# Optimization experiments

Measured on AMD Instinct MI355X. Metric: run time of the kernel, lower is better.

Reference implementation:

```python
import jax, jax.numpy as jnp
import numpy as np

B, H, W, C = 64, 32, 32, 256
HZ, WZ = 16, 16
N = 64          # hidden_dim = n_proposals
K = 3           # dynamic depthwise kernel size
EPS = 1e-5


def _layernorm(x, g, b):
    mu = jnp.mean(x, axis=-1, keepdims=True)
    var = jnp.var(x, axis=-1, keepdims=True)
    return (x - mu) * jax.lax.rsqrt(var + EPS) * g + b


def setup_inputs() -> dict:
    key = jax.random.key(0)
    ks = jax.random.split(key, 8)
    s = 0.02  # weight init scale
    return {
        "x_feat": jax.random.normal(ks[0], (B, H, W, C), jnp.float32),
        "z_feat": jax.random.normal(ks[1], (B, HZ, WZ, C), jnp.float32),
        "Wz": jax.random.normal(ks[2], (C, N), jnp.float32) * s,
        "bz": jnp.zeros((N,), jnp.float32),
        "Wx": jax.random.normal(ks[3], (C, N), jnp.float32) * s,
        "bx": jnp.zeros((N,), jnp.float32),
        "Wdyn": jax.random.normal(ks[4], (C, N + K), jnp.float32) * s,
        "bdyn": jnp.zeros((N + K,), jnp.float32),
        "g_norm": jnp.ones((C,), jnp.float32),
        "b_norm": jnp.zeros((C,), jnp.float32),
        "Wp": jax.random.normal(ks[5], (C, 1), jnp.float32) * s,
        "bp": jnp.zeros((1,), jnp.float32),
        "g_ln": jnp.ones((C,), jnp.float32),
        "b_ln": jnp.zeros((C,), jnp.float32),
    }


def _dysep_conv_atten(query, value, Wdyn, bdyn, g_norm, b_norm):
    # query, value: [B, N, C]
    dy = query @ Wdyn + bdyn                      # [B, N, N+K]
    w_depth = dy[:, :, :K]                        # [B, N, K] per-channel depthwise kernels
    w_point = dy[:, :, K:]                        # [B, N, N] per-sample pointwise (1x1) weights
    # depthwise conv along C with 'same' padding (torch conv1d = cross-correlation)
    vpad = jnp.pad(value, ((0, 0), (0, 0), (1, 1)))
    depth = (w_depth[..., 0:1] * vpad[:, :, 0:C]
             + w_depth[..., 1:2] * vpad[:, :, 1:C + 1]
             + w_depth[..., 2:3] * vpad[:, :, 2:C + 2])
    depth = jax.nn.relu(depth)                    # [B, N, C]
    point = jnp.einsum('bnm,bmc->bnc', w_point, depth)
    return _layernorm(point, g_norm, b_norm)


def reference(x_feat, z_feat, Wz, bz, Wx, bx, Wdyn, bdyn,
              g_norm, b_norm, Wp, bp, g_ln, b_ln):
    # kernels from template features (detached in the original: kernels.detach())
    z_core = z_feat @ Wz + bz                                   # [B,HZ,WZ,N]
    kernels = jnp.einsum('bhwn,bhwc->bnc', z_core, z_feat)      # [B,N,C]
    kernels = jax.lax.stop_gradient(kernels)

    x_n = x_feat @ Wx + bx                                      # [B,H,W,N]
    kernels_x = jnp.einsum('bhwn,bhwc->bnc', x_n, x_feat)       # [B,N,C]
    kernels_x = _dysep_conv_atten(kernels, kernels_x, Wdyn, bdyn, g_norm, b_norm)

    x_corr = jnp.einsum('bnc,bhwn->bhwc', kernels_x, x_n)       # [B,H,W,C]
    proto = kernels_x @ Wp + bp                                 # [B,N,1]
    tem = jax.nn.sigmoid(jnp.einsum('bnd,bnc->bdc', proto, kernels_x))  # [B,1,C]
    tem = tem[:, :, None, :]                                    # [B,1,1,C]
    x_corr = x_corr * tem

    return x_feat + jax.nn.relu(_layernorm(x_corr, g_ln, b_ln))
```

## Files before the change

kernel.cpp:

```cpp
#include <hip/hip_runtime.h>
#include <math.h>

#define EPSV 1e-5f

typedef __attribute__((ext_vector_type(8))) short short8;
typedef __attribute__((ext_vector_type(4))) float f32x4;

static __device__ __forceinline__ unsigned bfpack2(float lo, float hi) {
    union { float f; unsigned u; } a, b;
    a.f = lo; b.f = hi;
    unsigned ua = a.u + 0x7fffu + ((a.u >> 16) & 1u);
    unsigned ub = b.u + 0x7fffu + ((b.u >> 16) & 1u);
    return (ua >> 16) | (ub & 0xffff0000u);
}

__global__ __launch_bounds__(256) void gram(
    const float* __restrict__ Xx, const float* __restrict__ Xz,
    float* __restrict__ Gx, float* __restrict__ Gz,
    float* __restrict__ csx, float* __restrict__ csz)
{
    __shared__ __align__(16) unsigned short AT[64 * 72];
    __shared__ __align__(16) unsigned short BT[64 * 72];
    __shared__ float csr[256];
    int id = blockIdx.x;
    const float* X; float* G; float* cs; int P;
    if (id < 1024) { X = Xx; G = Gx; cs = csx; P = 1024; }
    else { id -= 1024; X = Xz; G = Gz; cs = csz; P = 256; }
    const int b = id & 63;
    const int tile = id >> 6;
    const int ci = tile >> 2, cj = tile & 3;
    const int nk = P >> 6;
    const int t = threadIdx.x;
    const int cl = t & 63, ph = t >> 6;
    const int w = t >> 6, quad = (t >> 4) & 3, lane16 = t & 15;
    const float* Xb = X + (long)b * P * 256;
    const float* Acol = Xb + ci * 64 + cl;
    const float* Bcol = Xb + cj * 64 + cl;
    const bool diag = (ci == cj);

    f32x4 acc[4] = {{0.f,0.f,0.f,0.f},{0.f,0.f,0.f,0.f},{0.f,0.f,0.f,0.f},{0.f,0.f,0.f,0.f}};
    float csum = 0.f;

    for (int kc = 0; kc < nk; ++kc) {
        const int p0 = kc * 64 + ph * 16;
        float va[16], vb[16];
#pragma unroll
        for (int k = 0; k < 16; ++k) va[k] = Acol[(long)(p0 + k) * 256];
        if (!diag) {
#pragma unroll
            for (int k = 0; k < 16; ++k) vb[k] = Bcol[(long)(p0 + k) * 256];
        } else {
#pragma unroll
            for (int k = 0; k < 16; ++k) { vb[k] = va[k]; csum += va[k]; }
        }
        uint4 a0, a1, b0, b1;
        a0.x = bfpack2(va[0], va[1]);   a0.y = bfpack2(va[2], va[3]);
        a0.z = bfpack2(va[4], va[5]);   a0.w = bfpack2(va[6], va[7]);
        a1.x = bfpack2(va[8], va[9]);   a1.y = bfpack2(va[10], va[11]);
        a1.z = bfpack2(va[12], va[13]); a1.w = bfpack2(va[14], va[15]);
        b0.x = bfpack2(vb[0], vb[1]);   b0.y = bfpack2(vb[2], vb[3]);
        b0.z = bfpack2(vb[4], vb[5]);   b0.w = bfpack2(vb[6], vb[7]);
        b1.x = bfpack2(vb[8], vb[9]);   b1.y = bfpack2(vb[10], vb[11]);
        b1.z = bfpack2(vb[12], vb[13]); b1.w = bfpack2(vb[14], vb[15]);
        __syncthreads();
        *(uint4*)&AT[cl * 72 + ph * 16]     = a0;
        *(uint4*)&AT[cl * 72 + ph * 16 + 8] = a1;
        *(uint4*)&BT[cl * 72 + ph * 16]     = b0;
        *(uint4*)&BT[cl * 72 + ph * 16 + 8] = b1;
        __syncthreads();
#pragma unroll
        for (int ks = 0; ks < 2; ++ks) {
            const int ko = ks * 32 + quad * 8;
            short8 bfrag = *(const short8*)&BT[(w * 16 + lane16) * 72 + ko];
#pragma unroll
            for (int mi = 0; mi < 4; ++mi) {
                short8 afrag = *(const short8*)&AT[(mi * 16 + lane16) * 72 + ko];
                acc[mi] = __builtin_amdgcn_mfma_f32_16x16x32_bf16(afrag, bfrag, acc[mi], 0, 0, 0);
            }
        }
    }
#pragma unroll
    for (int mi = 0; mi < 4; ++mi) {
        long row = (long)(b * 256 + ci * 64 + mi * 16 + quad * 4);
        int col = cj * 64 + w * 16 + lane16;
#pragma unroll
        for (int r = 0; r < 4; ++r)
            G[(row + r) * 256 + col] = acc[mi][r];
    }
    if (diag) {
        csr[ph * 64 + cl] = csum;
        __syncthreads();
        if (t < 64)
            cs[b * 256 + ci * 64 + t] = csr[t] + csr[64 + t] + csr[128 + t] + csr[192 + t];
    }
}

__global__ __launch_bounds__(256) void proj(
    const float* __restrict__ Gx, const float* __restrict__ csx,
    const float* __restrict__ Wx, const float* __restrict__ bx,
    float* __restrict__ kxr,
    const float* __restrict__ Gz, const float* __restrict__ csz,
    const float* __restrict__ Wz, const float* __restrict__ bz,
    float* __restrict__ kern)
{
    __shared__ __align__(16) unsigned short ATW[64 * 264];
    __shared__ __align__(16) unsigned short BTC[64 * 72];
    const int t = threadIdx.x;
    const int id = blockIdx.x;
    const int b = id & 63, s = id >> 6;
    const float *G, *cs, *W, *bias; float* O;
    if (s < 4) { G = Gx; cs = csx; W = Wx; bias = bx; O = kxr; }
    else       { G = Gz; cs = csz; W = Wz; bias = bz; O = kern; }
    const int ct = s & 3;
    const int n = t & 63, ph = t >> 6;
#pragma unroll
    for (int cc = 0; cc < 4; ++cc) {
        float v[16];
#pragma unroll
        for (int k = 0; k < 16; ++k) v[k] = W[(ph * 64 + cc * 16 + k) * 64 + n];
        uint4 p0, p1;
        p0.x = bfpack2(v[0], v[1]);   p0.y = bfpack2(v[2], v[3]);
        p0.z = bfpack2(v[4], v[5]);   p0.w = bfpack2(v[6], v[7]);
        p1.x = bfpack2(v[8], v[9]);   p1.y = bfpack2(v[10], v[11]);
        p1.z = bfpack2(v[12], v[13]); p1.w = bfpack2(v[14], v[15]);
        *(uint4*)&ATW[n * 264 + ph * 64 + cc * 16]     = p0;
        *(uint4*)&ATW[n * 264 + ph * 64 + cc * 16 + 8] = p1;
    }
    const int row = t >> 2, cq = t & 3;
    const int w = t >> 6, quad = (t >> 4) & 3, lane16 = t & 15;
    const float* Grow = G + ((long)(b * 256 + ct * 64 + row)) * 256 + cq * 16;
    f32x4 acc[4] = {{0.f,0.f,0.f,0.f},{0.f,0.f,0.f,0.f},{0.f,0.f,0.f,0.f},{0.f,0.f,0.f,0.f}};
    for (int kc = 0; kc < 4; ++kc) {
        float4 g0 = *(const float4*)(Grow + kc * 64 + 0);
        float4 g1 = *(const float4*)(Grow + kc * 64 + 4);
        float4 g2 = *(const float4*)(Grow + kc * 64 + 8);
        float4 g3 = *(const float4*)(Grow + kc * 64 + 12);
        uint4 pk0, pk1;
        pk0.x = bfpack2(g0.x, g0.y); pk0.y = bfpack2(g0.z, g0.w);
        pk0.z = bfpack2(g1.x, g1.y); pk0.w = bfpack2(g1.z, g1.w);
        pk1.x = bfpack2(g2.x, g2.y); pk1.y = bfpack2(g2.z, g2.w);
        pk1.z = bfpack2(g3.x, g3.y); pk1.w = bfpack2(g3.z, g3.w);
        __syncthreads();
        *(uint4*)&BTC[row * 72 + cq * 16]     = pk0;
        *(uint4*)&BTC[row * 72 + cq * 16 + 8] = pk1;
        __syncthreads();
#pragma unroll
        for (int ks = 0; ks < 2; ++ks) {
            const int ko = ks * 32 + quad * 8;
            short8 bfrag = *(const short8*)&BTC[(w * 16 + lane16) * 72 + ko];
#pragma unroll
            for (int mi = 0; mi < 4; ++mi) {
                short8 afrag = *(const short8*)&ATW[(mi * 16 + lane16) * 264 + kc * 64 + ko];
                acc[mi] = __builtin_amdgcn_mfma_f32_16x16x32_bf16(afrag, bfrag, acc[mi], 0, 0, 0);
            }
        }
    }
    const int col = ct * 64 + w * 16 + lane16;
    const float csv = cs[b * 256 + col];
#pragma unroll
    for (int mi = 0; mi < 4; ++mi) {
        const int nrow = mi * 16 + quad * 4;
#pragma unroll
        for (int r = 0; r < 4; ++r)
            O[((long)(b * 64 + nrow + r)) * 256 + col] = acc[mi][r] + bias[nrow + r] * csv;
    }
}

__global__ __launch_bounds__(256) void dy_all(
    const float* __restrict__ kern, const float* __restrict__ Wdyn,
    const float* __restrict__ bdyn, float* __restrict__ dyb)
{
    __shared__ float Ac[16 * 64];
    __shared__ float Wc[16 * 64];
    __shared__ float Wd3[48];
    const int b = blockIdx.x, t = threadIdx.x;
    const int tr = t >> 4, tc = t & 15;
    float acc[4][4];
#pragma unroll
    for (int j = 0; j < 4; ++j) {
        float bj = bdyn[3 + tc * 4 + j];
        acc[0][j] = bj; acc[1][j] = bj; acc[2][j] = bj; acc[3][j] = bj;
    }
    const int lr = t >> 2, lc = (t & 3) * 4;
    const int wl = t >> 4, wj = (t & 15) * 4;
    const int nwd = t / 3, jwd = t - nwd * 3;
    float wdacc = 0.f;
    float4 av = *(const float4*)(kern + ((long)(b * 64 + lr)) * 256 + lc);
    float w0 = Wdyn[wl * 67 + 3 + wj + 0];
    float w1 = Wdyn[wl * 67 + 3 + wj + 1];
    float w2 = Wdyn[wl * 67 + 3 + wj + 2];
    float w3 = Wdyn[wl * 67 + 3 + wj + 3];
    float wdr = (t < 48) ? Wdyn[(t / 3) * 67 + (t % 3)] : 0.f;

    for (int c0 = 0; c0 < 256; c0 += 16) {
        Ac[(lc+0)*64 + lr] = av.x; Ac[(lc+1)*64 + lr] = av.y;
        Ac[(lc+2)*64 + lr] = av.z; Ac[(lc+3)*64 + lr] = av.w;
        Wc[wl*64 + wj+0] = w0; Wc[wl*64 + wj+1] = w1;
        Wc[wl*64 + wj+2] = w2; Wc[wl*64 + wj+3] = w3;
        if (t < 48) Wd3[t] = wdr;
        __syncthreads();
        if (c0 + 16 < 256) {
            av = *(const float4*)(kern + ((long)(b * 64 + lr)) * 256 + c0 + 16 + lc);
            w0 = Wdyn[(c0 + 16 + wl) * 67 + 3 + wj + 0];
            w1 = Wdyn[(c0 + 16 + wl) * 67 + 3 + wj + 1];
            w2 = Wdyn[(c0 + 16 + wl) * 67 + 3 + wj + 2];
            w3 = Wdyn[(c0 + 16 + wl) * 67 + 3 + wj + 3];
            if (t < 48) wdr = Wdyn[(c0 + 16 + t / 3) * 67 + (t % 3)];
        }
#pragma unroll
        for (int cl = 0; cl < 16; ++cl) {
            float4 a = *(float4*)&Ac[cl * 64 + tr * 4];
            float4 w = *(float4*)&Wc[cl * 64 + tc * 4];
            acc[0][0]+=a.x*w.x; acc[0][1]+=a.x*w.y; acc[0][2]+=a.x*w.z; acc[0][3]+=a.x*w.w;
            acc[1][0]+=a.y*w.x; acc[1][1]+=a.y*w.y; acc[1][2]+=a.y*w.z; acc[1][3]+=a.y*w.w;
            acc[2][0]+=a.z*w.x; acc[2][1]+=a.z*w.y; acc[2][2]+=a.z*w.z; acc[2][3]+=a.z*w.w;
            acc[3][0]+=a.w*w.x; acc[3][1]+=a.w*w.y; acc[3][2]+=a.w*w.z; acc[3][3]+=a.w*w.w;
        }
        if (t < 192) {
#pragma unroll
            for (int cl = 0; cl < 16; ++cl)
                wdacc += Ac[cl * 64 + nwd] * Wd3[cl * 3 + jwd];
        }
        __syncthreads();
    }
#pragma unroll
    for (int i = 0; i < 4; ++i) {
        float4 o = make_float4(acc[i][0], acc[i][1], acc[i][2], acc[i][3]);
        *(float4*)(dyb + ((long)(b * 64 + tr * 4 + i)) * 68 + tc * 4) = o;
    }
    if (t < 192) dyb[((long)(b * 64 + nwd)) * 68 + 64 + jwd] = wdacc + bdyn[jwd];
}

__global__ __launch_bounds__(256) void depthpoint(
    const float* __restrict__ dyb, const float* __restrict__ v,
    const float* __restrict__ g, const float* __restrict__ Wp,
    float* __restrict__ point, float* __restrict__ partials)
{
    __shared__ float smem[13312];
    float* wpT = smem;
    float* wd3 = smem + 4352;
    float* vt  = smem + 4608;
    float* dep = smem + 8960;
    float* rs  = vt;

    const int t = threadIdx.x;
    const int b = blockIdx.y, ct = blockIdx.x, c0 = ct * 64;
    const int tr = t >> 4, tc = t & 15;

#pragma unroll
    for (int i = 0; i < 4; ++i) {
        int idx = t + i * 256; int n = idx >> 4, m0 = (idx & 15) * 4;
        float4 w4 = *(const float4*)(dyb + ((long)(b * 64 + n)) * 68 + m0);
        wpT[(m0+0)*68 + n] = w4.x; wpT[(m0+1)*68 + n] = w4.y;
        wpT[(m0+2)*68 + n] = w4.z; wpT[(m0+3)*68 + n] = w4.w;
    }
    if (t < 64) {
        long o = ((long)(b * 64 + t)) * 68 + 64;
        wd3[t*4+0] = dyb[o+0]; wd3[t*4+1] = dyb[o+1]; wd3[t*4+2] = dyb[o+2];
    }
    {
        int m = t >> 2, lc0 = (t & 3) * 17;
#pragma unroll
        for (int k = 0; k < 17; ++k) {
            int lc = lc0 + k;
            if (lc < 66) {
                int c = c0 - 1 + lc;
                vt[m * 68 + lc] = (c >= 0 && c < 256) ? v[((long)(b * 64 + m)) * 256 + c] : 0.f;
            }
        }
    }
    __syncthreads();
#pragma unroll
    for (int im = 0; im < 4; ++im) {
        int m = tr * 4 + im;
        float w0 = wd3[m*4+0], w1 = wd3[m*4+1], w2 = wd3[m*4+2];
#pragma unroll
        for (int jc = 0; jc < 4; ++jc) {
            int cl = tc * 4 + jc;
            float d = w0 * vt[m*68 + cl] + w1 * vt[m*68 + cl + 1] + w2 * vt[m*68 + cl + 2];
            dep[m*68 + cl] = fmaxf(d, 0.f);
        }
    }
    __syncthreads();
    float acc[4][4] = {};
#pragma unroll 16
    for (int m = 0; m < 64; ++m) {
        float4 a4 = *(float4*)&wpT[m * 68 + tr * 4];
        float4 d4 = *(float4*)&dep[m * 68 + tc * 4];
        acc[0][0]+=a4.x*d4.x; acc[0][1]+=a4.x*d4.y; acc[0][2]+=a4.x*d4.z; acc[0][3]+=a4.x*d4.w;
        acc[1][0]+=a4.y*d4.x; acc[1][1]+=a4.y*d4.y; acc[1][2]+=a4.y*d4.z; acc[1][3]+=a4.y*d4.w;
        acc[2][0]+=a4.z*d4.x; acc[2][1]+=a4.z*d4.y; acc[2][2]+=a4.z*d4.z; acc[2][3]+=a4.z*d4.w;
        acc[3][0]+=a4.w*d4.x; acc[3][1]+=a4.w*d4.y; acc[3][2]+=a4.w*d4.z; acc[3][3]+=a4.w*d4.w;
    }
    int cg = c0 + tc * 4;
    float4 g4  = *(const float4*)(g + cg);
    float4 wp4 = *(const float4*)(Wp + cg);
    float gw0 = g4.x*wp4.x, gw1 = g4.y*wp4.y, gw2 = g4.z*wp4.z, gw3 = g4.w*wp4.w;
#pragma unroll
    for (int i = 0; i < 4; ++i) {
        float4 o = make_float4(acc[i][0], acc[i][1], acc[i][2], acc[i][3]);
        *(float4*)(point + ((long)(b * 64 + tr * 4 + i)) * 256 + cg) = o;
        float s  = o.x + o.y + o.z + o.w;
        float s2 = o.x*o.x + o.y*o.y + o.z*o.z + o.w*o.w;
        float dg = o.x*gw0 + o.y*gw1 + o.z*gw2 + o.w*gw3;
        rs[0*1088 + (tr*4+i)*17 + tc] = s;
        rs[1*1088 + (tr*4+i)*17 + tc] = s2;
        rs[2*1088 + (tr*4+i)*17 + tc] = dg;
    }
    __syncthreads();
    if (t < 64) {
        float s = 0.f, s2 = 0.f, dg = 0.f;
#pragma unroll
        for (int j = 0; j < 16; ++j) {
            s  += rs[t*17 + j];
            s2 += rs[1088 + t*17 + j];
            dg += rs[2176 + t*17 + j];
        }
        long base = ((long)(b * 4 + ct)) * 192;
        partials[base + t]        = s;
        partials[base + 64 + t]   = s2;
        partials[base + 128 + t]  = dg;
    }
}

__global__ __launch_bounds__(256) void lntem(
    const float* __restrict__ partials, const float* __restrict__ point,
    const float* __restrict__ g, const float* __restrict__ bta,
    const float* __restrict__ Wp, const float* __restrict__ bp,
    float* __restrict__ murr, float* __restrict__ AB)
{
    __shared__ float sA[256], sB[256];
    __shared__ float wnv[64];
    __shared__ float tot[4];
    const int b = blockIdx.x, t = threadIdx.x;
    const int c = t;
    float gc = g[c], bc = bta[c], wpc = Wp[c];
    sA[t] = gc * wpc; sB[t] = bc * wpc;
    __syncthreads();
    for (int off = 128; off >= 1; off >>= 1) {
        if (t < off) { sA[t] += sA[t+off]; sB[t] += sB[t+off]; }
        __syncthreads();
    }
    if (t == 0) { tot[0] = sA[0]; tot[1] = sB[0] + bp[0]; }
    __syncthreads();
    float Sgw = tot[0], Sbw = tot[1];

    float protoe = 0.f, mu = 0.f, rr = 0.f;
    if (t < 64) {
        float S1 = 0.f, S2 = 0.f, Sdg = 0.f;
#pragma unroll
        for (int ct = 0; ct < 4; ++ct) {
            long o = ((long)(b * 4 + ct)) * 192;
            S1 += partials[o + t]; S2 += partials[o + 64 + t]; Sdg += partials[o + 128 + t];
        }
        mu = S1 * (1.f / 256.f);
        float var = S2 * (1.f / 256.f) - mu * mu;
        rr = rsqrtf(var + EPSV);
        protoe = rr * (Sdg - mu * Sgw) + Sbw;
        wnv[t] = protoe * rr;
        murr[b * 128 + 2*t]     = rr;
        murr[b * 128 + 2*t + 1] = -mu * rr;
    }
    __syncthreads();
    sA[t] = (t < 64) ? protoe * rr * mu : 0.f;
    sB[t] = (t < 64) ? protoe : 0.f;
    __syncthreads();
    for (int off = 128; off >= 1; off >>= 1) {
        if (t < off) { sA[t] += sA[t+off]; sB[t] += sB[t+off]; }
        __syncthreads();
    }
    if (t == 0) { tot[2] = sA[0]; tot[3] = sB[0]; }
    __syncthreads();
    float Bv = tot[2], Sv = tot[3];

    const float* pcol = point + (long)b * 64 * 256 + c;
    float a0 = 0.f, a1 = 0.f, a2 = 0.f, a3 = 0.f;
#pragma unroll
    for (int n = 0; n < 64; n += 4) {
        a0 += wnv[n+0] * pcol[(n+0) * 256];
        a1 += wnv[n+1] * pcol[(n+1) * 256];
        a2 += wnv[n+2] * pcol[(n+2) * 256];
        a3 += wnv[n+3] * pcol[(n+3) * 256];
    }
    float accA = a0 + a1 + a2 + a3;
    float x = gc * (accA - Bv) + bc * Sv;
    float temv = 1.f / (1.f + expf(-x));
    AB[b * 512 + c]       = gc * temv;
    AB[b * 512 + 256 + c] = bc * temv;
}

__global__ __launch_bounds__(256) void buildM(
    const float* __restrict__ point, const float* __restrict__ murr,
    const float* __restrict__ AB, const float* __restrict__ Wx,
    const float* __restrict__ bx,
    unsigned short* __restrict__ MT, float* __restrict__ svec)
{
    __shared__ float ks_s[64 * 68];
    __shared__ float wt_s[64 * 68];
    const int t = threadIdx.x;
    const int id = blockIdx.x;
    const int b = id & 63, mt = id >> 6;
    {
        const int n = t >> 2, q = t & 3;
        const float rn = murr[b * 128 + 2 * n], qn = murr[b * 128 + 2 * n + 1];
        const float* prow = point + ((long)(b * 64 + n)) * 256 + mt * 64 + q * 16;
        const float* Arow = AB + b * 512 + mt * 64 + q * 16;
#pragma unroll
        for (int j = 0; j < 4; ++j) {
            float4 p4 = *(const float4*)(prow + j * 4);
            float4 A4 = *(const float4*)(Arow + j * 4);
            float4 B4 = *(const float4*)(Arow + 256 + j * 4);
            float4 kv;
            kv.x = (p4.x * rn + qn) * A4.x + B4.x;
            kv.y = (p4.y * rn + qn) * A4.y + B4.y;
            kv.z = (p4.z * rn + qn) * A4.z + B4.z;
            kv.w = (p4.w * rn + qn) * A4.w + B4.w;
            *(float4*)&ks_s[n * 68 + q * 16 + j * 4] = kv;
        }
    }
    __syncthreads();
    if (t < 64) {
        float sv = 0.f;
#pragma unroll
        for (int n2 = 0; n2 < 64; ++n2) sv += bx[n2] * ks_s[n2 * 68 + t];
        svec[b * 256 + mt * 64 + t] = sv;
    }
    const int tr = t >> 4, tc = t & 15;
    const int nw = t & 63, ph = t >> 6;
    for (int cc = 0; cc < 4; ++cc) {
        float wv[16];
#pragma unroll
        for (int k = 0; k < 16; ++k) wv[k] = Wx[(cc * 64 + ph * 16 + k) * 64 + nw];
        __syncthreads();
#pragma unroll
        for (int k = 0; k < 16; ++k) wt_s[nw * 68 + ph * 16 + k] = wv[k];
        __syncthreads();
        float a2[4][4] = {};
#pragma unroll 16
        for (int n2 = 0; n2 < 64; ++n2) {
            float4 a4 = *(float4*)&ks_s[n2 * 68 + tr * 4];
            float4 w4 = *(float4*)&wt_s[n2 * 68 + tc * 4];
            a2[0][0]+=a4.x*w4.x; a2[0][1]+=a4.x*w4.y; a2[0][2]+=a4.x*w4.z; a2[0][3]+=a4.x*w4.w;
            a2[1][0]+=a4.y*w4.x; a2[1][1]+=a4.y*w4.y; a2[1][2]+=a4.y*w4.z; a2[1][3]+=a4.y*w4.w;
            a2[2][0]+=a4.z*w4.x; a2[2][1]+=a4.z*w4.y; a2[2][2]+=a4.z*w4.z; a2[2][3]+=a4.z*w4.w;
            a2[3][0]+=a4.w*w4.x; a2[3][1]+=a4.w*w4.y; a2[3][2]+=a4.w*w4.z; a2[3][3]+=a4.w*w4.w;
        }
#pragma unroll
        for (int i = 0; i < 4; ++i) {
            uint2 pk;
            pk.x = bfpack2(a2[i][0], a2[i][1]);
            pk.y = bfpack2(a2[i][2], a2[i][3]);
            *(uint2*)&MT[((long)(b * 256 + mt * 64 + tr * 4 + i)) * 256 + cc * 64 + tc * 4] = pk;
        }
    }
}

__global__ __launch_bounds__(256) void final2(
    const float* __restrict__ xf, const unsigned short* __restrict__ MT,
    const float* __restrict__ svec, const float* __restrict__ g,
    const float* __restrict__ bt, float* __restrict__ out)
{
    __shared__ __align__(16) float SlArr[64 * 132];
    __shared__ float red1[256], red2[256];
    __shared__ float muS[64], rrS[64];
    unsigned short* XT = (unsigned short*)SlArr;
    float* Sl = SlArr;
    const int t = threadIdx.x;
    const int id = blockIdx.x;
    const int b = id & 63, pt = id >> 6;
    const int w = t >> 6, quad = (t >> 4) & 3, lane16 = t & 15;
    const float* Xb = xf + ((long)(b * 1024 + pt * 64)) * 256;
    {
        const int p = t >> 2, q = t & 3;
#pragma unroll
        for (int j = 0; j < 4; ++j)
#pragma unroll
            for (int i = 0; i < 4; ++i) {
                const int c = j * 64 + q * 16 + i * 4;
                float4 v = *(const float4*)(Xb + (long)p * 256 + c);
                uint2 pk;
                pk.x = bfpack2(v.x, v.y);
                pk.y = bfpack2(v.z, v.w);
                *(uint2*)&XT[p * 264 + c] = pk;
            }
    }
    __syncthreads();
    f32x4 acc[4][4] = {};
    const unsigned short* Mb = MT + (long)b * 65536;
    for (int ks = 0; ks < 8; ++ks) {
        const int ko = ks * 32 + quad * 8;
        short8 bf4[4], af4[4];
#pragma unroll
        for (int ni = 0; ni < 4; ++ni)
            bf4[ni] = *(const short8*)(Mb + (long)(w * 64 + ni * 16 + lane16) * 256 + ko);
#pragma unroll
        for (int mi = 0; mi < 4; ++mi)
            af4[mi] = *(const short8*)&XT[(mi * 16 + lane16) * 264 + ko];
#pragma unroll
        for (int mi = 0; mi < 4; ++mi)
#pragma unroll
            for (int ni = 0; ni < 4; ++ni)
                acc[mi][ni] = __builtin_amdgcn_mfma_f32_16x16x32_bf16(af4[mi], bf4[ni], acc[mi][ni], 0, 0, 0);
    }
    float sv4[4];
#pragma unroll
    for (int ni = 0; ni < 4; ++ni) sv4[ni] = svec[b * 256 + w * 64 + ni * 16 + lane16];
#pragma unroll
    for (int mi = 0; mi < 4; ++mi)
#pragma unroll
        for (int r = 0; r < 4; ++r) {
            float s1 = 0.f, s2 = 0.f;
#pragma unroll
            for (int ni = 0; ni < 4; ++ni) {
                float v = acc[mi][ni][r] + sv4[ni];
                acc[mi][ni][r] = v;
                s1 += v; s2 += v * v;
            }
#pragma unroll
            for (int m = 1; m <= 8; m <<= 1) {
                s1 += __shfl_xor(s1, m);
                s2 += __shfl_xor(s2, m);
            }
            if (lane16 == 0) {
                red1[(mi * 16 + quad * 4 + r) * 4 + w] = s1;
                red2[(mi * 16 + quad * 4 + r) * 4 + w] = s2;
            }
        }
    __syncthreads();
    if (t < 64) {
        float sa = red1[t*4] + red1[t*4+1] + red1[t*4+2] + red1[t*4+3];
        float sb = red2[t*4] + red2[t*4+1] + red2[t*4+2] + red2[t*4+3];
        float m = sa * (1.f / 256.f);
        muS[t] = m;
        rrS[t] = rsqrtf(sb * (1.f / 256.f) - m * m + EPSV);
    }
#pragma unroll
    for (int h = 0; h < 2; ++h) {
        __syncthreads();
        if ((w >> 1) == h) {
            const int chalf = (w & 1) * 64;
#pragma unroll
            for (int mi = 0; mi < 4; ++mi)
#pragma unroll
                for (int ni = 0; ni < 4; ++ni)
#pragma unroll
                    for (int r = 0; r < 4; ++r)
                        Sl[(mi * 16 + quad * 4 + r) * 132 + chalf + ni * 16 + lane16] = acc[mi][ni][r];
        }
        __syncthreads();
        {
            const int p = t >> 2, q = t & 3;
            const float m = muS[p], rr = rrS[p];
            const long grow = ((long)(b * 1024 + pt * 64 + p)) * 256;
#pragma unroll
            for (int j = 0; j < 8; ++j) {
                const int cl = q * 32 + j * 4;
                const int c = h * 128 + cl;
                float4 a  = *(float4*)&Sl[p * 132 + cl];
                float4 g4 = *(const float4*)(g + c);
                float4 b4 = *(const float4*)(bt + c);
                float4 xv = *(const float4*)(xf + grow + c);
                float4 o;
                o.x = xv.x + fmaxf((a.x - m) * rr * g4.x + b4.x, 0.f);
                o.y = xv.y + fmaxf((a.y - m) * rr * g4.y + b4.y, 0.f);
                o.z = xv.z + fmaxf((a.z - m) * rr * g4.z + b4.z, 0.f);
                o.w = xv.w + fmaxf((a.w - m) * rr * g4.w + b4.w, 0.f);
                *(float4*)(out + grow + c) = o;
            }
        }
    }
}

extern "C" void kernel_launch(void* const* d_in, const int* in_sizes, int n_in,
                              void* d_out, int out_size, void* d_ws, size_t ws_size,
                              hipStream_t stream)
{
    (void)in_sizes; (void)n_in; (void)out_size; (void)ws_size;
    const float* x_feat = (const float*)d_in[0];
    const float* z_feat = (const float*)d_in[1];
    const float* Wz     = (const float*)d_in[2];
    const float* bz     = (const float*)d_in[3];
    const float* Wx     = (const float*)d_in[4];
    const float* bx     = (const float*)d_in[5];
    const float* Wdyn   = (const float*)d_in[6];
    const float* bdyn   = (const float*)d_in[7];
    const float* g_norm = (const float*)d_in[8];
    const float* b_norm = (const float*)d_in[9];
    const float* Wp     = (const float*)d_in[10];
    const float* bp     = (const float*)d_in[11];
    const float* g_ln   = (const float*)d_in[12];
    const float* b_ln   = (const float*)d_in[13];
    float* out = (float*)d_out;

    float* ws       = (float*)d_ws;
    float* Gx       = ws;
    float* Gz       = Gx + 4194304;
    float* kern     = Gz + 4194304;
    float* kxr      = kern + 1048576;
    float* point    = kxr + 1048576;
    float* dyb      = point + 1048576;
    float* partials = dyb + 278528;
    float* murr     = partials + 49152;
    float* AB       = murr + 8192;
    float* csx      = AB + 32768;
    float* csz      = csx + 16384;
    float* svec     = csz + 16384;
    unsigned short* MT = (unsigned short*)(svec + 16384);

    gram<<<2048, 256, 0, stream>>>(x_feat, z_feat, Gx, Gz, csx, csz);
    proj<<<512, 256, 0, stream>>>(Gx, csx, Wx, bx, kxr, Gz, csz, Wz, bz, kern);
    dy_all<<<64, 256, 0, stream>>>(kern, Wdyn, bdyn, dyb);
    depthpoint<<<dim3(4, 64), 256, 0, stream>>>(dyb, kxr, g_norm, Wp, point, partials);
    lntem<<<64, 256, 0, stream>>>(partials, point, g_norm, b_norm, Wp, bp, murr, AB);
    buildM<<<256, 256, 0, stream>>>(point, murr, AB, Wx, bx, MT, svec);
    final2<<<1024, 256, 0, stream>>>(x_feat, MT, svec, g_ln, b_ln, out);
}
```

Baseline: 299.2 us.

## Exploit Gram symmetry with larger 128x128 tiles and halve final2 row tile

The Gram kernel now computes 128x128 tiles and only the three upper-triangular blocks per batch, mirroring the off-diagonal block into the lower half. Loads switch from strided scalar column reads to row-wise float4 loads. This removes the redundant work on symmetric blocks and reduces memory traffic. The final kernel processes 32 rows per block instead of 64 and launches twice as many blocks, trading per-block MFMA reuse of MT for more parallelism and less LDS per block. The mirrored transposed store is uncoalesced.

```diff
diff --git a/kernel.cpp b/kernel.cpp
--- a/kernel.cpp
+++ b/kernel.cpp
@@ -19,79 +19,111 @@
     float* __restrict__ Gx, float* __restrict__ Gz,
     float* __restrict__ csx, float* __restrict__ csz)
 {
-    __shared__ __align__(16) unsigned short AT[64 * 72];
-    __shared__ __align__(16) unsigned short BT[64 * 72];
-    __shared__ float csr[256];
+    __shared__ __align__(16) unsigned short AT[128 * 72];
+    __shared__ __align__(16) unsigned short BT[128 * 72];
+    __shared__ float csr[8 * 128];
     int id = blockIdx.x;
     const float* X; float* G; float* cs; int P;
-    if (id < 1024) { X = Xx; G = Gx; cs = csx; P = 1024; }
-    else { id -= 1024; X = Xz; G = Gz; cs = csz; P = 256; }
+    if (id < 192) { X = Xx; G = Gx; cs = csx; P = 1024; }
+    else { id -= 192; X = Xz; G = Gz; cs = csz; P = 256; }
     const int b = id & 63;
     const int tile = id >> 6;
-    const int ci = tile >> 2, cj = tile & 3;
+    const int ci = (tile == 1) ? 1 : 0;
+    const int cj = (tile == 0) ? 0 : 1;
+    const bool diag = (tile < 2);
     const int nk = P >> 6;
     const int t = threadIdx.x;
-    const int cl = t & 63, ph = t >> 6;
-    const int w = t >> 6, quad = (t >> 4) & 3, lane16 = t & 15;
+    const int cq = (t & 31) * 4;
+    const int ph = t >> 5;
     const float* Xb = X + (long)b * P * 256;
-    const float* Acol = Xb + ci * 64 + cl;
-    const float* Bcol = Xb + cj * 64 + cl;
-    const bool diag = (ci == cj);
-
-    f32x4 acc[4] = {{0.f,0.f,0.f,0.f},{0.f,0.f,0.f,0.f},{0.f,0.f,0.f,0.f},{0.f,0.f,0.f,0.f}};
-    float csum = 0.f;
+
+    const int w = t >> 6;
+    const int wr = w >> 1, wc = w & 1;
+    const int quad = (t >> 4) & 3, lane16 = t & 15;
+
+    f32x4 acc[4][4] = {};
+    float csA[4] = {0.f, 0.f, 0.f, 0.f};
 
     for (int kc = 0; kc < nk; ++kc) {
-        const int p0 = kc * 64 + ph * 16;
-        float va[16], vb[16];
-#pragma unroll
-        for (int k = 0; k < 16; ++k) va[k] = Acol[(long)(p0 + k) * 256];
+        const int p0 = kc * 64 + ph * 8;
+        float4 va[8], vb[8];
+#pragma unroll
+        for (int k = 0; k < 8; ++k)
+            va[k] = *(const float4*)(Xb + (long)(p0 + k) * 256 + ci * 128 + cq);
         if (!diag) {
 #pragma unroll
-            for (int k = 0; k < 16; ++k) vb[k] = Bcol[(long)(p0 + k) * 256];
-        } else {
-#pragma unroll
-            for (int k = 0; k < 16; ++k) { vb[k] = va[k]; csum += va[k]; }
-        }
-        uint4 a0, a1, b0, b1;
-        a0.x = bfpack2(va[0], va[1]);   a0.y = bfpack2(va[2], va[3]);
-        a0.z = bfpack2(va[4], va[5]);   a0.w = bfpack2(va[6], va[7]);
-        a1.x = bfpack2(va[8], va[9]);   a1.y = bfpack2(va[10], va[11]);
-        a1.z = bfpack2(va[12], va[13]); a1.w = bfpack2(va[14], va[15]);
-        b0.x = bfpack2(vb[0], vb[1]);   b0.y = bfpack2(vb[2], vb[3]);
-        b0.z = bfpack2(vb[4], vb[5]);   b0.w = bfpack2(vb[6], vb[7]);
-        b1.x = bfpack2(vb[8], vb[9]);   b1.y = bfpack2(vb[10], vb[11]);
-        b1.z = bfpack2(vb[12], vb[13]); b1.w = bfpack2(vb[14], vb[15]);
-        __syncthreads();
-        *(uint4*)&AT[cl * 72 + ph * 16]     = a0;
-        *(uint4*)&AT[cl * 72 + ph * 16 + 8] = a1;
-        *(uint4*)&BT[cl * 72 + ph * 16]     = b0;
-        *(uint4*)&BT[cl * 72 + ph * 16 + 8] = b1;
-        __syncthreads();
+            for (int k = 0; k < 8; ++k)
+                vb[k] = *(const float4*)(Xb + (long)(p0 + k) * 256 + cj * 128 + cq);
+        }
+        __syncthreads();
+#pragma unroll
+        for (int j = 0; j < 4; ++j) {
+            uint4 pk;
+            pk.x = bfpack2(((const float*)&va[0])[j], ((const float*)&va[1])[j]);
+            pk.y = bfpack2(((const float*)&va[2])[j], ((const float*)&va[3])[j]);
+            pk.z = bfpack2(((const float*)&va[4])[j], ((const float*)&va[5])[j]);
+            pk.w = bfpack2(((const float*)&va[6])[j], ((const float*)&va[7])[j]);
+            *(uint4*)&AT[(cq + j) * 72 + ph * 8] = pk;
+            if (diag) {
+                csA[j] += ((const float*)&va[0])[j] + ((const float*)&va[1])[j]
+                        + ((const float*)&va[2])[j] + ((const float*)&va[3])[j]
+                        + ((const float*)&va[4])[j] + ((const float*)&va[5])[j]
+                        + ((const float*)&va[6])[j] + ((const float*)&va[7])[j];
+            }
+        }
+        if (!diag) {
+#pragma unroll
+            for (int j = 0; j < 4; ++j) {
+                uint4 pk;
+                pk.x = bfpack2(((const float*)&vb[0])[j], ((const float*)&vb[1])[j]);
+                pk.y = bfpack2(((const float*)&vb[2])[j], ((const float*)&vb[3])[j]);
+                pk.z = bfpack2(((const float*)&vb[4])[j], ((const float*)&vb[5])[j]);
+                pk.w = bfpack2(((const float*)&vb[6])[j], ((const float*)&vb[7])[j]);
+                *(uint4*)&BT[(cq + j) * 72 + ph * 8] = pk;
+            }
+        }
+        __syncthreads();
+        const unsigned short* Br = diag ? AT : BT;
 #pragma unroll
         for (int ks = 0; ks < 2; ++ks) {
             const int ko = ks * 32 + quad * 8;
-            short8 bfrag = *(const short8*)&BT[(w * 16 + lane16) * 72 + ko];
+            short8 bfrag[4];
+#pragma unroll
+            for (int ni = 0; ni < 4; ++ni)
+                bfrag[ni] = *(const short8*)&Br[(wc * 64 + ni * 16 + lane16) * 72 + ko];
 #pragma unroll
             for (int mi = 0; mi < 4; ++mi) {
-                short8 afrag = *(const short8*)&AT[(mi * 16 + lane16) * 72 + ko];
-                acc[mi] = __builtin_amdgcn_mfma_f32_16x16x32_bf16(afrag, bfrag, acc[mi], 0, 0, 0);
+                short8 afrag = *(const short8*)&AT[(wr * 64 + mi * 16 + lane16) * 72 + ko];
+#pragma unroll
+                for (int ni = 0; ni < 4; ++ni)
+                    acc[mi][ni] = __builtin_amdgcn_mfma_f32_16x16x32_bf16(afrag, bfrag[ni], acc[mi][ni], 0, 0, 0);
             }
         }
     }
 #pragma unroll
     for (int mi = 0; mi < 4; ++mi) {
-        long row = (long)(b * 256 + ci * 64 + mi * 16 + quad * 4);
-        int col = cj * 64 + w * 16 + lane16;
-#pragma unroll
-        for (int r = 0; r < 4; ++r)
-            G[(row + r) * 256 + col] = acc[mi][r];
+        const int rbase = ci * 128 + wr * 64 + mi * 16 + quad * 4;
+#pragma unroll
+        for (int ni = 0; ni < 4; ++ni) {
+            const int col = cj * 128 + wc * 64 + ni * 16 + lane16;
+#pragma unroll
+            for (int r = 0; r < 4; ++r) {
+                G[((long)(b * 256 + rbase + r)) * 256 + col] = acc[mi][ni][r];
+                if (!diag)
+                    G[((long)(b * 256 + col)) * 256 + rbase + r] = acc[mi][ni][r];
+            }
+        }
     }
     if (diag) {
-        csr[ph * 64 + cl] = csum;
-        __syncthreads();
-        if (t < 64)
-            cs[b * 256 + ci * 64 + t] = csr[t] + csr[64 + t] + csr[128 + t] + csr[192 + t];
+#pragma unroll
+        for (int j = 0; j < 4; ++j) csr[ph * 128 + cq + j] = csA[j];
+        __syncthreads();
+        if (t < 128) {
+            float s = 0.f;
+#pragma unroll
+            for (int k = 0; k < 8; ++k) s += csr[k * 128 + t];
+            cs[b * 256 + ci * 128 + t] = s;
+        }
     }
 }
 
@@ -460,61 +492,59 @@
     const float* __restrict__ svec, const float* __restrict__ g,
     const float* __restrict__ bt, float* __restrict__ out)
 {
-    __shared__ __align__(16) float SlArr[64 * 132];
-    __shared__ float red1[256], red2[256];
-    __shared__ float muS[64], rrS[64];
+    __shared__ __align__(16) float SlArr[32 * 132];
+    __shared__ float red1[128], red2[128];
+    __shared__ float muS[32], rrS[32];
     unsigned short* XT = (unsigned short*)SlArr;
     float* Sl = SlArr;
     const int t = threadIdx.x;
     const int id = blockIdx.x;
     const int b = id & 63, pt = id >> 6;
     const int w = t >> 6, quad = (t >> 4) & 3, lane16 = t & 15;
-    const float* Xb = xf + ((long)(b * 1024 + pt * 64)) * 256;
+    const float* Xb = xf + ((long)(b * 1024 + pt * 32)) * 256;
     {
-        const int p = t >> 2, q = t & 3;
-#pragma unroll
-        for (int j = 0; j < 4; ++j)
-#pragma unroll
-            for (int i = 0; i < 4; ++i) {
-                const int c = j * 64 + q * 16 + i * 4;
-                float4 v = *(const float4*)(Xb + (long)p * 256 + c);
-                uint2 pk;
-                pk.x = bfpack2(v.x, v.y);
-                pk.y = bfpack2(v.z, v.w);
-                *(uint2*)&XT[p * 264 + c] = pk;
-            }
-    }
-    __syncthreads();
-    f32x4 acc[4][4] = {};
+        const int p = t >> 3, q = t & 7;
+#pragma unroll
+        for (int i = 0; i < 8; ++i) {
+            const int c = q * 32 + i * 4;
+            float4 v = *(const float4*)(Xb + (long)p * 256 + c);
+            uint2 pk;
+            pk.x = bfpack2(v.x, v.y);
+            pk.y = bfpack2(v.z, v.w);
+            *(uint2*)&XT[p * 264 + c] = pk;
+        }
+    }
+    __syncthreads();
+    f32x4 acc[2][4] = {};
     const unsigned short* Mb = MT + (long)b * 65536;
     for (int ks = 0; ks < 8; ++ks) {
         const int ko = ks * 32 + quad * 8;
-        short8 bf4[4], af4[4];
+        short8 bf4[4], af2[2];
 #pragma unroll
         for (int ni = 0; ni < 4; ++ni)
             bf4[ni] = *(const short8*)(Mb + (long)(w * 64 + ni * 16 + lane16) * 256 + ko);
 #pragma unroll
-        for (int mi = 0; mi < 4; ++mi)
-            af4[mi] = *(const short8*)&XT[(mi * 16 + lane16) * 264 + ko];
-#pragma unroll
-        for (int mi = 0; mi < 4; ++mi)
+        for (int mi = 0; mi < 2; ++mi)
+            af2[mi] = *(const short8*)&XT[(mi * 16 + lane16) * 264 + ko];
+#pragma unroll
+        for (int mi = 0; mi < 2; ++mi)
 #pragma unroll
             for (int ni = 0; ni < 4; ++ni)
-                acc[mi][ni] = __builtin_amdgcn_mfma_f32_16x16x32_bf16(af4[mi], bf4[ni], acc[mi][ni], 0, 0, 0);
+                acc[mi][ni] = __builtin_amdgcn_mfma_f32_16x16x32_bf16(af2[mi], bf4[ni], acc[mi][ni], 0, 0, 0);
     }
     float sv4[4];
 #pragma unroll
     for (int ni = 0; ni < 4; ++ni) sv4[ni] = svec[b * 256 + w * 64 + ni * 16 + lane16];
 #pragma unroll
-    for (int mi = 0; mi < 4; ++mi)
+    for (int mi = 0; mi < 2; ++mi)
 #pragma unroll
         for (int r = 0; r < 4; ++r) {
             float s1 = 0.f, s2 = 0.f;
 #pragma unroll
             for (int ni = 0; ni < 4; ++ni) {
-                float v = acc[mi][ni][r] + sv4[ni];
-                acc[mi][ni][r] = v;
-                s1 += v; s2 += v * v;
+                float v2 = acc[mi][ni][r] + sv4[ni];
+                acc[mi][ni][r] = v2;
+                s1 += v2; s2 += v2 * v2;
             }
 #pragma unroll
             for (int m = 1; m <= 8; m <<= 1) {
@@ -527,7 +557,7 @@
             }
         }
     __syncthreads();
-    if (t < 64) {
+    if (t < 32) {
         float sa = red1[t*4] + red1[t*4+1] + red1[t*4+2] + red1[t*4+3];
         float sb = red2[t*4] + red2[t*4+1] + red2[t*4+2] + red2[t*4+3];
         float m = sa * (1.f / 256.f);
@@ -540,7 +570,7 @@
         if ((w >> 1) == h) {
             const int chalf = (w & 1) * 64;
 #pragma unroll
-            for (int mi = 0; mi < 4; ++mi)
+            for (int mi = 0; mi < 2; ++mi)
 #pragma unroll
                 for (int ni = 0; ni < 4; ++ni)
 #pragma unroll
@@ -549,12 +579,12 @@
         }
         __syncthreads();
         {
-            const int p = t >> 2, q = t & 3;
+            const int p = t >> 3, q = t & 7;
             const float m = muS[p], rr = rrS[p];
-            const long grow = ((long)(b * 1024 + pt * 64 + p)) * 256;
-#pragma unroll
-            for (int j = 0; j < 8; ++j) {
-                const int cl = q * 32 + j * 4;
+            const long grow = ((long)(b * 1024 + pt * 32 + p)) * 256;
+#pragma unroll
+            for (int j = 0; j < 4; ++j) {
+                const int cl = q * 16 + j * 4;
                 const int c = h * 128 + cl;
                 float4 a  = *(float4*)&Sl[p * 132 + cl];
                 float4 g4 = *(const float4*)(g + c);
@@ -607,11 +637,11 @@
     float* svec     = csz + 16384;
     unsigned short* MT = (unsigned short*)(svec + 16384);
 
-    gram<<<2048, 256, 0, stream>>>(x_feat, z_feat, Gx, Gz, csx, csz);
+    gram<<<384, 256, 0, stream>>>(x_feat, z_feat, Gx, Gz, csx, csz);
     proj<<<512, 256, 0, stream>>>(Gx, csx, Wx, bx, kxr, Gz, csz, Wz, bz, kern);
     dy_all<<<64, 256, 0, stream>>>(kern, Wdyn, bdyn, dyb);
     depthpoint<<<dim3(4, 64), 256, 0, stream>>>(dyb, kxr, g_norm, Wp, point, partials);
     lntem<<<64, 256, 0, stream>>>(partials, point, g_norm, b_norm, Wp, bp, murr, AB);
     buildM<<<256, 256, 0, stream>>>(point, murr, AB, Wx, bx, MT, svec);
-    final2<<<1024, 256, 0, stream>>>(x_feat, MT, svec, g_ln, b_ln, out);
-}
+    final2<<<2048, 256, 0, stream>>>(x_feat, MT, svec, g_ln, b_ln, out);
+}
```

Result: no change. 297.8 us (-0.5%).
